# Performance work log

Measured on AMD Instinct MI355X. Metric: run time of the kernel, lower is better.

The kernel has to match this reference:

```python
import jax, jax.numpy as jnp
import numpy as np

B_, T_, L_, M_, H_, F_ = 16, 2048, 128, 256, 512, 1024
EPS = 1e-5


def _init_reservoir(h, rng):
    # orthogonal matrix scaled inside the unit disk for a stable linear recurrence
    q, _ = np.linalg.qr(rng.standard_normal((h, h)).astype(np.float32))
    return jnp.asarray(0.95 * q, dtype=jnp.float32)


def setup_inputs() -> dict:
    key = jax.random.key(0)
    ks = jax.random.split(key, 8)
    rng = np.random.default_rng(0)
    s = lambda fan_in: 1.0 / np.sqrt(fan_in)
    return {
        "x": jax.random.normal(ks[0], (B_, T_, L_), dtype=jnp.float32),
        "We": jax.random.uniform(ks[1], (L_, M_), jnp.float32, -s(L_), s(L_)),
        "be": jnp.zeros((M_,), jnp.float32),
        "Wb": jax.random.uniform(ks[2], (M_, H_), jnp.float32, -s(M_), s(M_)),
        "A": _init_reservoir(H_, rng),
        "Wr": jax.random.uniform(ks[3], (L_, H_), jnp.float32, -s(L_), s(L_)),
        "br": jnp.zeros((H_,), jnp.float32),
        "ln_g": jnp.ones((H_,), jnp.float32),
        "ln_b": jnp.zeros((H_,), jnp.float32),
        "W1": jax.random.uniform(ks[4], (H_, F_), jnp.float32, -s(H_), s(H_)),
        "b1": jnp.zeros((F_,), jnp.float32),
        "W2": jax.random.uniform(ks[5], (F_, H_), jnp.float32, -s(F_), s(F_)),
        "b2": jnp.zeros((H_,), jnp.float32),
    }


def reference(x, We, be, Wb, A, Wr, br, ln_g, ln_b, W1, b1, W2, b2):
    # encoder + B projection, batched over all timesteps: [B,T,H]
    Bu = (x @ We + be) @ Wb

    # sequential linear recurrence h_t = h_{t-1} @ A + Bu_t, h_0 = Bu_0
    def step(h, bu_t):
        h = h @ A + bu_t
        return h, h

    h0 = jnp.zeros((x.shape[0], A.shape[0]), x.dtype)
    _, Hs = jax.lax.scan(step, h0, jnp.swapaxes(Bu, 0, 1))  # [T,B,H]
    H_seq = jnp.swapaxes(Hs, 0, 1)  # [B,T,H]

    # residual + layer norm
    z = H_seq + (x @ Wr + br)
    mu = jnp.mean(z, axis=-1, keepdims=True)
    var = jnp.mean(jnp.square(z - mu), axis=-1, keepdims=True)
    zn = (z - mu) * jax.lax.rsqrt(var + EPS) * ln_g + ln_b

    # MLP on last timestep
    h_last = zn[:, -1, :]
    out = jax.nn.relu(h_last @ W1 + b1) @ W2 + b2
    return out
```

## Files before the change

### kernel.cpp

```cpp
#include <hip/hip_runtime.h>

#define B_  16
#define T_  2048
#define L_  128
#define H_  512
#define F_  1024
#define EPS 1e-5f

#define GP   68
#define GSM  (64 * GP * 2)

#define SS_P (512 * 512)

struct Job {
    const float* A; const float* Aaux; const float* B; const float* Add;
    float* C; float* C2;
    int M, lda, kLen, nbx, nrt, amode, nsA, ssA, nsB, ssB;
};

__device__ __forceinline__ float4 jloadA(const Job& jb, int gr, int gk) {
    if (jb.amode == 1) {
        if (gr < 128)  return *(const float4*)(jb.A + (long)gr * jb.lda + gk);
        if (gr == 128) return *(const float4*)(jb.Aaux + gk);
        return make_float4(0.f, 0.f, 0.f, 0.f);
    }
    if (jb.amode == 3) {
        int b = gr & 15, lag = gr >> 4;
        return *(const float4*)(jb.A + ((long)b * T_ + (T_ - 1 - lag)) * L_ + gk);
    }
    int row = gr;
    if (jb.amode == 2) row = ((gr >> 4) << 5) + 16 + (gr & 15);
    else if (gr >= jb.M) return make_float4(0.f, 0.f, 0.f, 0.f);
    const float* p = jb.A + (long)row * 512 + gk;
    float4 s = *(const float4*)p;
    for (int q = 1; q < jb.nsA; ++q) {
        float4 t = *(const float4*)(p + (long)q * jb.ssA);
        s.x += t.x; s.y += t.y; s.z += t.z; s.w += t.w;
    }
    return s;
}

__device__ __forceinline__ float4 jloadB(const Job& jb, int gk, int c) {
    const float* p = jb.B + (long)gk * 512 + c;
    float4 s = *(const float4*)p;
    for (int q = 1; q < jb.nsB; ++q) {
        float4 t = *(const float4*)(p + (long)q * jb.ssB);
        s.x += t.x; s.y += t.y; s.z += t.z; s.w += t.w;
    }
    return s;
}

__device__ __forceinline__ void g64run(float* sm, const Job& jb, int rel) {
    float* As = sm;
    float* Bs = sm + 64 * GP;
    const int tid = threadIdx.x, tx = tid & 15, ty = tid >> 4;
    const int bx = rel % jb.nbx;
    const int r  = rel / jb.nbx;
    const int by = r % jb.nrt;
    const int kc = r / jb.nrt;
    const int row0 = by * 64, col0 = bx * 64, kOff = kc * jb.kLen;

    float4 pa[4], pb[4];
#pragma unroll
    for (int t = 0; t < 4; ++t) {
        int f = tid + t * 256;
        pa[t] = jloadA(jb, row0 + (f >> 4), kOff + (f & 15) * 4);
        pb[t] = jloadB(jb, kOff + (f >> 4), col0 + (f & 15) * 4);
    }
    float acc[4][4] = {};
    for (int k0 = 0; k0 < jb.kLen; k0 += 64) {
        __syncthreads();
#pragma unroll
        for (int t = 0; t < 4; ++t) {
            int f = tid + t * 256;
            int ar = f >> 4, ak = (f & 15) * 4;
            As[(ak + 0) * GP + ar] = pa[t].x;
            As[(ak + 1) * GP + ar] = pa[t].y;
            As[(ak + 2) * GP + ar] = pa[t].z;
            As[(ak + 3) * GP + ar] = pa[t].w;
            *(float4*)&Bs[(f >> 4) * GP + (f & 15) * 4] = pb[t];
        }
        __syncthreads();
        int kn = k0 + 64;
        if (kn < jb.kLen) {
#pragma unroll
            for (int t = 0; t < 4; ++t) {
                int f = tid + t * 256;
                pa[t] = jloadA(jb, row0 + (f >> 4), kOff + kn + (f & 15) * 4);
                pb[t] = jloadB(jb, kOff + kn + (f >> 4), col0 + (f & 15) * 4);
            }
        }
#pragma unroll
        for (int kk = 0; kk < 64; ++kk) {
            float4 ra = *(float4*)&As[kk * GP + ty * 4];
            float4 rb = *(float4*)&Bs[kk * GP + tx * 4];
            acc[0][0] = fmaf(ra.x, rb.x, acc[0][0]);
            acc[0][1] = fmaf(ra.x, rb.y, acc[0][1]);
            acc[0][2] = fmaf(ra.x, rb.z, acc[0][2]);
            acc[0][3] = fmaf(ra.x, rb.w, acc[0][3]);
            acc[1][0] = fmaf(ra.y, rb.x, acc[1][0]);
            acc[1][1] = fmaf(ra.y, rb.y, acc[1][1]);
            acc[1][2] = fmaf(ra.y, rb.z, acc[1][2]);
            acc[1][3] = fmaf(ra.y, rb.w, acc[1][3]);
            acc[2][0] = fmaf(ra.z, rb.x, acc[2][0]);
            acc[2][1] = fmaf(ra.z, rb.y, acc[2][1]);
            acc[2][2] = fmaf(ra.z, rb.z, acc[2][2]);
            acc[2][3] = fmaf(ra.z, rb.w, acc[2][3]);
            acc[3][0] = fmaf(ra.w, rb.x, acc[3][0]);
            acc[3][1] = fmaf(ra.w, rb.y, acc[3][1]);
            acc[3][2] = fmaf(ra.w, rb.z, acc[3][2]);
            acc[3][3] = fmaf(ra.w, rb.w, acc[3][3]);
        }
    }
    long coff = (long)kc * jb.M * 512;
#pragma unroll
    for (int i = 0; i < 4; ++i) {
        int rr = row0 + ty * 4 + i;
        if (rr >= jb.M) continue;
        int c = col0 + tx * 4;
        float4 v = make_float4(acc[i][0], acc[i][1], acc[i][2], acc[i][3]);
        if (jb.amode == 2 && kc == 0) {
            long prow = (long)(((rr >> 4) << 5) + (rr & 15)) * 512;
            const float* ap = jb.Add + prow + c;
            for (int q = 0; q < jb.nsA; ++q) {
                float4 ad = *(const float4*)(ap + (long)q * jb.ssA);
                v.x += ad.x; v.y += ad.y; v.z += ad.z; v.w += ad.w;
            }
        }
        if (jb.amode == 3) {
            v.x += jb.Aaux[c]; v.y += jb.Aaux[c + 1];
            v.z += jb.Aaux[c + 2]; v.w += jb.Aaux[c + 3];
        }
        if (jb.amode == 1 && rr == 128)
            *(float4*)(jb.C2 + c) = v;
        else
            *(float4*)(jb.C + coff + (long)rr * 512 + c) = v;
    }
}

struct Pack { Job j[3]; int n0, n1; };

__global__ __launch_bounds__(256) void gstage(Pack p) {
    __shared__ float sm[GSM];
    int b = blockIdx.x, rel;
    const Job* jb;
    if (b < p.n0) { jb = &p.j[0]; rel = b; }
    else if (b < p.n0 + p.n1) { jb = &p.j[1]; rel = b - p.n0; }
    else { jb = &p.j[2]; rel = b - p.n0 - p.n1; }
    if (jb->amode == 9) {
        const float4* src = (const float4*)jb->A;
        float4* dst = (float4*)jb->C;
        int ss4 = jb->ssA >> 2;
        for (int i = rel * 256 + threadIdx.x; i < SS_P / 4; i += 32 * 256) {
            float4 s = src[i];
            for (int q = 1; q < jb->nsA; ++q) {
                float4 t = src[i + q * ss4];
                s.x += t.x; s.y += t.y; s.z += t.z; s.w += t.w;
            }
            dst[i] = s;
        }
        return;
    }
    g64run(sm, *jb, rel);
}

struct TP {
    const float* Y5s; const float* P32; const float* P64; const float* P96s;
    const float* x; const float* Wr; const float* zn; const float* W1;
    const float* h1p; const float* b1; const float* W2;
    float* outp; int nbx, kLen;
};

template <int MODE>
__device__ __forceinline__ float4 ta4(const TP& tp, int b, int gk) {
    if (MODE == 0) {
        if (gk < 1536) {
            int seg = gk >> 9, inner = gk & 511;
            const float* p = tp.Y5s + (long)((seg + 1) * 16 + b) * 512 + inner;
            float4 s = *(const float4*)p;
#pragma unroll
            for (int q = 1; q < 8; ++q) {
                float4 t = *(const float4*)(p + (long)q * 64 * 512);
                s.x += t.x; s.y += t.y; s.z += t.z; s.w += t.w;
            }
            return s;
        }
        return *(const float4*)(tp.x + ((long)b * T_ + T_ - 1) * L_ + gk - 1536);
    } else if (MODE == 1) {
        return *(const float4*)(tp.zn + (long)b * H_ + gk);
    } else {
        float4 s = *(const float4*)(tp.b1 + gk);
#pragma unroll
        for (int q = 0; q < 4; ++q) {
            float4 h = *(const float4*)(tp.h1p + (long)q * 16 * F_ + (long)b * F_ + gk);
            s.x += h.x; s.y += h.y; s.z += h.z; s.w += h.w;
        }
        return make_float4(fmaxf(s.x, 0.f), fmaxf(s.y, 0.f),
                           fmaxf(s.z, 0.f), fmaxf(s.w, 0.f));
    }
}

template <int MODE>
__device__ __forceinline__ float4 tb4(const TP& tp, int kr, int c) {
    if (MODE == 0) {
        if (kr < 512)  return *(const float4*)(tp.P32 + (long)kr * 512 + c);
        if (kr < 1024) return *(const float4*)(tp.P64 + (long)(kr - 512) * 512 + c);
        if (kr < 1536) {
            const float* p = tp.P96s + (long)(kr - 1024) * 512 + c;
            float4 s = *(const float4*)p;
#pragma unroll
            for (int q = 1; q < 4; ++q) {
                float4 t = *(const float4*)(p + (long)q * SS_P);
                s.x += t.x; s.y += t.y; s.z += t.z; s.w += t.w;
            }
            return s;
        }
        return *(const float4*)(tp.Wr + (long)(kr - 1536) * 512 + c);
    } else if (MODE == 1) {
        return *(const float4*)(tp.W1 + (long)kr * F_ + c);
    } else {
        return *(const float4*)(tp.W2 + (long)kr * H_ + c);
    }
}

template <int MODE>
__global__ __launch_bounds__(256) void tstage(TP tp) {
    constexpr int LDC = (MODE == 1) ? F_ : H_;
    __shared__ float sm[64 * 20 + 64 * 68];
    float* As = sm;
    float* Bs = sm + 64 * 20;
    const int tid = threadIdx.x, tx = tid & 15, ty = tid >> 4;
    const int kc = blockIdx.x / tp.nbx;
    const int col0 = (blockIdx.x % tp.nbx) * 64;
    const int kOff = kc * tp.kLen;

    float4 pa, pb[4];
    pa = ta4<MODE>(tp, ty, kOff + tx * 4);
#pragma unroll
    for (int t = 0; t < 4; ++t) {
        int f = tid + t * 256;
        pb[t] = tb4<MODE>(tp, kOff + (f >> 4), col0 + (f & 15) * 4);
    }
    float acc[4] = {};
    for (int k0 = 0; k0 < tp.kLen; k0 += 64) {
        __syncthreads();
        {
            int kk = tx * 4;
            As[(kk + 0) * 20 + ty] = pa.x;
            As[(kk + 1) * 20 + ty] = pa.y;
            As[(kk + 2) * 20 + ty] = pa.z;
            As[(kk + 3) * 20 + ty] = pa.w;
        }
#pragma unroll
        for (int t = 0; t < 4; ++t) {
            int f = tid + t * 256;
            *(float4*)&Bs[(f >> 4) * 68 + (f & 15) * 4] = pb[t];
        }
        __syncthreads();
        int kn = k0 + 64;
        if (kn < tp.kLen) {
            pa = ta4<MODE>(tp, ty, kOff + kn + tx * 4);
#pragma unroll
            for (int t = 0; t < 4; ++t) {
                int f = tid + t * 256;
                pb[t] = tb4<MODE>(tp, kOff + kn + (f >> 4), col0 + (f & 15) * 4);
            }
        }
#pragma unroll
        for (int kk = 0; kk < 64; ++kk) {
            float ra = As[kk * 20 + ty];
            float4 rb = *(float4*)&Bs[kk * 68 + tx * 4];
            acc[0] = fmaf(ra, rb.x, acc[0]);
            acc[1] = fmaf(ra, rb.y, acc[1]);
            acc[2] = fmaf(ra, rb.z, acc[2]);
            acc[3] = fmaf(ra, rb.w, acc[3]);
        }
    }
    float* dst = tp.outp + (long)kc * 16 * LDC + (long)ty * LDC + col0 + tx * 4;
    *(float4*)dst = make_float4(acc[0], acc[1], acc[2], acc[3]);
}

__global__ __launch_bounds__(256) void zln(
    const float* __restrict__ zp, const float* __restrict__ Y5s,
    const float* __restrict__ br, const float* __restrict__ lng,
    const float* __restrict__ lnb, float* __restrict__ zn)
{
    __shared__ float red1[4], red2[4];
    const int b = blockIdx.x, tid = threadIdx.x;
    float z[2];
#pragma unroll
    for (int jj = 0; jj < 2; ++jj) {
        int c = tid + jj * 256;
        float s = br[c];
#pragma unroll
        for (int q = 0; q < 13; ++q) s += zp[(long)q * 16 * H_ + (long)b * H_ + c];
#pragma unroll
        for (int q = 0; q < 8; ++q) s += Y5s[(long)q * 64 * 512 + (long)b * 512 + c];
        z[jj] = s;
    }
    float s1 = z[0] + z[1];
    float s2 = z[0] * z[0] + z[1] * z[1];
#pragma unroll
    for (int off = 32; off > 0; off >>= 1) {
        s1 += __shfl_down(s1, off, 64);
        s2 += __shfl_down(s2, off, 64);
    }
    int wid = tid >> 6, lane = tid & 63;
    if (lane == 0) { red1[wid] = s1; red2[wid] = s2; }
    __syncthreads();
    float S1 = red1[0] + red1[1] + red1[2] + red1[3];
    float S2 = red2[0] + red2[1] + red2[2] + red2[3];
    float mu  = S1 * (1.0f / H_);
    float var = S2 * (1.0f / H_) - mu * mu;
    float rs  = rsqrtf(var + EPS);
#pragma unroll
    for (int jj = 0; jj < 2; ++jj) {
        int c = tid + jj * 256;
        zn[(long)b * H_ + c] = (z[jj] - mu) * rs * lng[c] + lnb[c];
    }
}

__global__ __launch_bounds__(256) void ored(
    const float* __restrict__ op, const float* __restrict__ b2,
    float* __restrict__ out)
{
    int b = blockIdx.x >> 1;
    int c = (blockIdx.x & 1) * 256 + threadIdx.x;
    float s = b2[c];
#pragma unroll
    for (int q = 0; q < 8; ++q) s += op[(long)q * 16 * H_ + (long)b * H_ + c];
    out[(long)b * H_ + c] = s;
}

extern "C" void kernel_launch(void* const* d_in, const int* in_sizes, int n_in,
                              void* d_out, int out_size, void* d_ws, size_t ws_size,
                              hipStream_t stream) {
    const float* x    = (const float*)d_in[0];
    const float* We   = (const float*)d_in[1];
    const float* be   = (const float*)d_in[2];
    const float* Wb   = (const float*)d_in[3];
    const float* Amat = (const float*)d_in[4];
    const float* Wr   = (const float*)d_in[5];
    const float* br   = (const float*)d_in[6];
    const float* lng  = (const float*)d_in[7];
    const float* lnb  = (const float*)d_in[8];
    const float* W1   = (const float*)d_in[9];
    const float* b1   = (const float*)d_in[10];
    const float* W2   = (const float*)d_in[11];
    const float* b2   = (const float*)d_in[12];
    float* out = (float*)d_out;

    float* ws   = (float*)d_ws;
    float* Wc   = ws;
    float* bc   = Wc + 128 * 512;
    float* U0   = bc + 512;
    float* Y1s  = U0 + 2048 * 512;
    float* Y2s  = Y1s + 2 * 1024 * 512;
    float* Y3s  = Y2s + 2 * 512 * 512;
    float* Y4s  = Y3s + 4 * 256 * 512;
    float* Y5s  = Y4s + 4 * 128 * 512;
    float* P2s  = Y5s + 8 * 64 * 512;
    float* P4s  = P2s + 4 * SS_P;
    float* P8s  = P4s + 4 * SS_P;
    float* P16s = P8s + 4 * SS_P;
    float* P32s = P16s + 4 * SS_P;
    float* P64s = P32s + 4 * SS_P;
    float* P96s = P64s + 4 * SS_P;
    float* P2d  = P96s + 4 * SS_P;
    float* P4d  = P2d + SS_P;
    float* P8d  = P4d + SS_P;
    float* P16d = P8d + SS_P;
    float* P32d = P16d + SS_P;
    float* P64d = P32d + SS_P;
    float* zp   = P64d + SS_P;
    float* zn   = zp + 13 * B_ * H_;
    float* h1p  = zn + B_ * H_;
    float* op   = h1p + 4 * B_ * F_;

    Job dummy = {}; dummy.amode = 9; dummy.nsA = 1; dummy.ssA = 4;
    dummy.A = Wc; dummy.C = Wc;

    {
        Pack p; p.j[2] = dummy;
        p.j[0] = {We, be, Wb, nullptr, Wc, bc, 129, 256, 256, 8, 3, 1, 1, 0, 1, 0};
        p.j[1] = {Amat, nullptr, Amat, nullptr, P2s, nullptr, 512, 512, 128, 8, 8, 0, 1, 0, 1, 0};
        p.n0 = 24; p.n1 = 256;
        gstage<<<280, 256, 0, stream>>>(p);
    }
    {
        Pack p;
        p.j[0] = {x, bc, Wc, nullptr, U0, nullptr, 2048, 0, 128, 8, 32, 3, 1, 0, 1, 0};
        p.j[1] = {P2s, nullptr, P2s, nullptr, P4s, nullptr, 512, 512, 128, 8, 8, 0, 4, SS_P, 4, SS_P};
        p.j[2] = {P2s, nullptr, nullptr, nullptr, P2d, nullptr, 512, 512, 64, 1, 1, 9, 4, SS_P, 1, 0};
        p.n0 = 256; p.n1 = 256;
        gstage<<<544, 256, 0, stream>>>(p);
    }
    {
        Pack p;
        p.j[0] = {U0, nullptr, Amat, U0, Y1s, nullptr, 1024, 512, 256, 8, 16, 2, 1, 0, 1, 0};
        p.j[1] = {P4s, nullptr, P4s, nullptr, P8s, nullptr, 512, 512, 128, 8, 8, 0, 4, SS_P, 4, SS_P};
        p.j[2] = {P4s, nullptr, nullptr, nullptr, P4d, nullptr, 512, 512, 64, 1, 1, 9, 4, SS_P, 1, 0};
        p.n0 = 256; p.n1 = 256;
        gstage<<<544, 256, 0, stream>>>(p);
    }
    {
        Pack p;
        p.j[0] = {Y1s, nullptr, P2d, Y1s, Y2s, nullptr, 512, 512, 256, 8, 8, 2, 2, 1024 * 512, 1, 0};
        p.j[1] = {P8s, nullptr, P8s, nullptr, P16s, nullptr, 512, 512, 128, 8, 8, 0, 4, SS_P, 4, SS_P};
        p.j[2] = {P8s, nullptr, nullptr, nullptr, P8d, nullptr, 512, 512, 64, 1, 1, 9, 4, SS_P, 1, 0};
        p.n0 = 128; p.n1 = 256;
        gstage<<<416, 256, 0, stream>>>(p);
    }
    {
        Pack p;
        p.j[0] = {Y2s, nullptr, P4d, Y2s, Y3s, nullptr, 256, 512, 128, 8, 4, 2, 2, 512 * 512, 1, 0};
        p.j[1] = {P16s, nullptr, P16s, nullptr, P32s, nullptr, 512, 512, 128, 8, 8, 0, 4, SS_P, 4, SS_P};
        p.j[2] = {P16s, nullptr, nullptr, nullptr, P16d, nullptr, 512, 512, 64, 1, 1, 9, 4, SS_P, 1, 0};
        p.n0 = 128; p.n1 = 256;
        gstage<<<416, 256, 0, stream>>>(p);
    }
    {
        Pack p;
        p.j[0] = {Y3s, nullptr, P8d, Y3s, Y4s, nullptr, 128, 512, 128, 8, 2, 2, 4, 256 * 512, 1, 0};
        p.j[1] = {P32s, nullptr, P32s, nullptr, P64s, nullptr, 512, 512, 128, 8, 8, 0, 4, SS_P, 4, SS_P};
        p.j[2] = {P32s, nullptr, nullptr, nullptr, P32d, nullptr, 512, 512, 64, 1, 1, 9, 4, SS_P, 1, 0};
        p.n0 = 64; p.n1 = 256;
        gstage<<<352, 256, 0, stream>>>(p);
    }
    {
        Pack p;
        p.j[0] = {Y4s, nullptr, P16d, Y4s, Y5s, nullptr, 64, 512, 64, 8, 1, 2, 4, 128 * 512, 1, 0};
        p.j[1] = {P32d, nullptr, P64s, nullptr, P96s, nullptr, 512, 512, 128, 8, 8, 0, 1, 0, 4, SS_P};
        p.j[2] = {P64s, nullptr, nullptr, nullptr, P64d, nullptr, 512, 512, 64, 1, 1, 9, 4, SS_P, 1, 0};
        p.n0 = 64; p.n1 = 256;
        gstage<<<352, 256, 0, stream>>>(p);
    }
    TP tp;
    tp.Y5s = Y5s; tp.P32 = P32d; tp.P64 = P64d; tp.P96s = P96s;
    tp.x = x; tp.Wr = Wr; tp.zn = zn; tp.W1 = W1; tp.h1p = h1p;
    tp.b1 = b1; tp.W2 = W2;

    { TP t = tp; t.outp = zp; t.nbx = 8; t.kLen = 128;
      tstage<0><<<104, 256, 0, stream>>>(t); }
    zln<<<16, 256, 0, stream>>>(zp, Y5s, br, lng, lnb, zn);
    { TP t = tp; t.outp = h1p; t.nbx = 16; t.kLen = 128;
      tstage<1><<<64, 256, 0, stream>>>(t); }
    { TP t = tp; t.outp = op; t.nbx = 8; t.kLen = 128;
      tstage<2><<<64, 256, 0, stream>>>(t); }
    ored<<<32, 256, 0, stream>>>(op, b2, out);
}
```

Measured before the change: 342.8 us.

## Drop split-K for matrix-power chain and double split-K in tail GEMMs

The A-power squaring GEMMs (P2, P4, ..., P96) now each run as one full-K job with 64 blocks, where before they used 4-way split-K with partial buffers. That removes the separate reduction jobs and the multi-slice summation on every operand load, which shortens gstage and the Pack struct. The tail GEMMs (tstage 0/1/2) go from K chunks of 128 to 64, doubling their block counts, and the downstream reductions (zln, tstage<2> loads, ored) now sum twice as many partials. The trade-off is fewer blocks and longer serial K loops in the critical power chain, in exchange for less memory traffic and fewer reduction passes.

```diff
diff --git a/kernel.cpp b/kernel.cpp
--- a/kernel.cpp
+++ b/kernel.cpp
@@ -10,12 +10,10 @@
 #define GP   68
 #define GSM  (64 * GP * 2)
 
-#define SS_P (512 * 512)
-
 struct Job {
     const float* A; const float* Aaux; const float* B; const float* Add;
     float* C; float* C2;
-    int M, lda, kLen, nbx, nrt, amode, nsA, ssA, nsB, ssB;
+    int M, lda, kLen, nbx, nrt, amode, nsA, ssA;
 };
 
 __device__ __forceinline__ float4 jloadA(const Job& jb, int gr, int gk) {
@@ -35,16 +33,6 @@
     float4 s = *(const float4*)p;
     for (int q = 1; q < jb.nsA; ++q) {
         float4 t = *(const float4*)(p + (long)q * jb.ssA);
-        s.x += t.x; s.y += t.y; s.z += t.z; s.w += t.w;
-    }
-    return s;
-}
-
-__device__ __forceinline__ float4 jloadB(const Job& jb, int gk, int c) {
-    const float* p = jb.B + (long)gk * 512 + c;
-    float4 s = *(const float4*)p;
-    for (int q = 1; q < jb.nsB; ++q) {
-        float4 t = *(const float4*)(p + (long)q * jb.ssB);
         s.x += t.x; s.y += t.y; s.z += t.z; s.w += t.w;
     }
     return s;
@@ -65,7 +53,7 @@
     for (int t = 0; t < 4; ++t) {
         int f = tid + t * 256;
         pa[t] = jloadA(jb, row0 + (f >> 4), kOff + (f & 15) * 4);
-        pb[t] = jloadB(jb, kOff + (f >> 4), col0 + (f & 15) * 4);
+        pb[t] = *(const float4*)(jb.B + (long)(kOff + (f >> 4)) * 512 + col0 + (f & 15) * 4);
     }
     float acc[4][4] = {};
     for (int k0 = 0; k0 < jb.kLen; k0 += 64) {
@@ -87,7 +75,8 @@
             for (int t = 0; t < 4; ++t) {
                 int f = tid + t * 256;
                 pa[t] = jloadA(jb, row0 + (f >> 4), kOff + kn + (f & 15) * 4);
-                pb[t] = jloadB(jb, kOff + kn + (f >> 4), col0 + (f & 15) * 4);
+                pb[t] = *(const float4*)(jb.B + (long)(kOff + kn + (f >> 4)) * 512 +
+                                         col0 + (f & 15) * 4);
             }
         }
 #pragma unroll
@@ -138,34 +127,17 @@
     }
 }
 
-struct Pack { Job j[3]; int n0, n1; };
+struct Pack { Job j[2]; int n0; };
 
 __global__ __launch_bounds__(256) void gstage(Pack p) {
     __shared__ float sm[GSM];
-    int b = blockIdx.x, rel;
-    const Job* jb;
-    if (b < p.n0) { jb = &p.j[0]; rel = b; }
-    else if (b < p.n0 + p.n1) { jb = &p.j[1]; rel = b - p.n0; }
-    else { jb = &p.j[2]; rel = b - p.n0 - p.n1; }
-    if (jb->amode == 9) {
-        const float4* src = (const float4*)jb->A;
-        float4* dst = (float4*)jb->C;
-        int ss4 = jb->ssA >> 2;
-        for (int i = rel * 256 + threadIdx.x; i < SS_P / 4; i += 32 * 256) {
-            float4 s = src[i];
-            for (int q = 1; q < jb->nsA; ++q) {
-                float4 t = src[i + q * ss4];
-                s.x += t.x; s.y += t.y; s.z += t.z; s.w += t.w;
-            }
-            dst[i] = s;
-        }
-        return;
-    }
-    g64run(sm, *jb, rel);
+    int b = blockIdx.x;
+    if (b < p.n0) g64run(sm, p.j[0], b);
+    else          g64run(sm, p.j[1], b - p.n0);
 }
 
 struct TP {
-    const float* Y5s; const float* P32; const float* P64; const float* P96s;
+    const float* Y5s; const float* P32; const float* P64; const float* P96;
     const float* x; const float* Wr; const float* zn; const float* W1;
     const float* h1p; const float* b1; const float* W2;
     float* outp; int nbx, kLen;
@@ -191,7 +163,7 @@
     } else {
         float4 s = *(const float4*)(tp.b1 + gk);
 #pragma unroll
-        for (int q = 0; q < 4; ++q) {
+        for (int q = 0; q < 8; ++q) {
             float4 h = *(const float4*)(tp.h1p + (long)q * 16 * F_ + (long)b * F_ + gk);
             s.x += h.x; s.y += h.y; s.z += h.z; s.w += h.w;
         }
@@ -205,16 +177,7 @@
     if (MODE == 0) {
         if (kr < 512)  return *(const float4*)(tp.P32 + (long)kr * 512 + c);
         if (kr < 1024) return *(const float4*)(tp.P64 + (long)(kr - 512) * 512 + c);
-        if (kr < 1536) {
-            const float* p = tp.P96s + (long)(kr - 1024) * 512 + c;
-            float4 s = *(const float4*)p;
-#pragma unroll
-            for (int q = 1; q < 4; ++q) {
-                float4 t = *(const float4*)(p + (long)q * SS_P);
-                s.x += t.x; s.y += t.y; s.z += t.z; s.w += t.w;
-            }
-            return s;
-        }
+        if (kr < 1536) return *(const float4*)(tp.P96 + (long)(kr - 1024) * 512 + c);
         return *(const float4*)(tp.Wr + (long)(kr - 1536) * 512 + c);
     } else if (MODE == 1) {
         return *(const float4*)(tp.W1 + (long)kr * F_ + c);
@@ -293,7 +256,7 @@
         int c = tid + jj * 256;
         float s = br[c];
 #pragma unroll
-        for (int q = 0; q < 13; ++q) s += zp[(long)q * 16 * H_ + (long)b * H_ + c];
+        for (int q = 0; q < 26; ++q) s += zp[(long)q * 16 * H_ + (long)b * H_ + c];
 #pragma unroll
         for (int q = 0; q < 8; ++q) s += Y5s[(long)q * 64 * 512 + (long)b * 512 + c];
         z[jj] = s;
@@ -328,7 +291,7 @@
     int c = (blockIdx.x & 1) * 256 + threadIdx.x;
     float s = b2[c];
 #pragma unroll
-    for (int q = 0; q < 8; ++q) s += op[(long)q * 16 * H_ + (long)b * H_ + c];
+    for (int q = 0; q < 16; ++q) s += op[(long)q * 16 * H_ + (long)b * H_ + c];
     out[(long)b * H_ + c] = s;
 }
 
@@ -350,102 +313,87 @@
     const float* b2   = (const float*)d_in[12];
     float* out = (float*)d_out;
 
-    float* ws   = (float*)d_ws;
-    float* Wc   = ws;
-    float* bc   = Wc + 128 * 512;
-    float* U0   = bc + 512;
-    float* Y1s  = U0 + 2048 * 512;
-    float* Y2s  = Y1s + 2 * 1024 * 512;
-    float* Y3s  = Y2s + 2 * 512 * 512;
-    float* Y4s  = Y3s + 4 * 256 * 512;
-    float* Y5s  = Y4s + 4 * 128 * 512;
-    float* P2s  = Y5s + 8 * 64 * 512;
-    float* P4s  = P2s + 4 * SS_P;
-    float* P8s  = P4s + 4 * SS_P;
-    float* P16s = P8s + 4 * SS_P;
-    float* P32s = P16s + 4 * SS_P;
-    float* P64s = P32s + 4 * SS_P;
-    float* P96s = P64s + 4 * SS_P;
-    float* P2d  = P96s + 4 * SS_P;
-    float* P4d  = P2d + SS_P;
-    float* P8d  = P4d + SS_P;
-    float* P16d = P8d + SS_P;
-    float* P32d = P16d + SS_P;
-    float* P64d = P32d + SS_P;
-    float* zp   = P64d + SS_P;
-    float* zn   = zp + 13 * B_ * H_;
-    float* h1p  = zn + B_ * H_;
-    float* op   = h1p + 4 * B_ * F_;
-
-    Job dummy = {}; dummy.amode = 9; dummy.nsA = 1; dummy.ssA = 4;
-    dummy.A = Wc; dummy.C = Wc;
-
-    {
-        Pack p; p.j[2] = dummy;
-        p.j[0] = {We, be, Wb, nullptr, Wc, bc, 129, 256, 256, 8, 3, 1, 1, 0, 1, 0};
-        p.j[1] = {Amat, nullptr, Amat, nullptr, P2s, nullptr, 512, 512, 128, 8, 8, 0, 1, 0, 1, 0};
-        p.n0 = 24; p.n1 = 256;
-        gstage<<<280, 256, 0, stream>>>(p);
-    }
-    {
-        Pack p;
-        p.j[0] = {x, bc, Wc, nullptr, U0, nullptr, 2048, 0, 128, 8, 32, 3, 1, 0, 1, 0};
-        p.j[1] = {P2s, nullptr, P2s, nullptr, P4s, nullptr, 512, 512, 128, 8, 8, 0, 4, SS_P, 4, SS_P};
-        p.j[2] = {P2s, nullptr, nullptr, nullptr, P2d, nullptr, 512, 512, 64, 1, 1, 9, 4, SS_P, 1, 0};
-        p.n0 = 256; p.n1 = 256;
-        gstage<<<544, 256, 0, stream>>>(p);
-    }
-    {
-        Pack p;
-        p.j[0] = {U0, nullptr, Amat, U0, Y1s, nullptr, 1024, 512, 256, 8, 16, 2, 1, 0, 1, 0};
-        p.j[1] = {P4s, nullptr, P4s, nullptr, P8s, nullptr, 512, 512, 128, 8, 8, 0, 4, SS_P, 4, SS_P};
-        p.j[2] = {P4s, nullptr, nullptr, nullptr, P4d, nullptr, 512, 512, 64, 1, 1, 9, 4, SS_P, 1, 0};
-        p.n0 = 256; p.n1 = 256;
-        gstage<<<544, 256, 0, stream>>>(p);
-    }
-    {
-        Pack p;
-        p.j[0] = {Y1s, nullptr, P2d, Y1s, Y2s, nullptr, 512, 512, 256, 8, 8, 2, 2, 1024 * 512, 1, 0};
-        p.j[1] = {P8s, nullptr, P8s, nullptr, P16s, nullptr, 512, 512, 128, 8, 8, 0, 4, SS_P, 4, SS_P};
-        p.j[2] = {P8s, nullptr, nullptr, nullptr, P8d, nullptr, 512, 512, 64, 1, 1, 9, 4, SS_P, 1, 0};
-        p.n0 = 128; p.n1 = 256;
-        gstage<<<416, 256, 0, stream>>>(p);
-    }
-    {
-        Pack p;
-        p.j[0] = {Y2s, nullptr, P4d, Y2s, Y3s, nullptr, 256, 512, 128, 8, 4, 2, 2, 512 * 512, 1, 0};
-        p.j[1] = {P16s, nullptr, P16s, nullptr, P32s, nullptr, 512, 512, 128, 8, 8, 0, 4, SS_P, 4, SS_P};
-        p.j[2] = {P16s, nullptr, nullptr, nullptr, P16d, nullptr, 512, 512, 64, 1, 1, 9, 4, SS_P, 1, 0};
-        p.n0 = 128; p.n1 = 256;
-        gstage<<<416, 256, 0, stream>>>(p);
-    }
-    {
-        Pack p;
-        p.j[0] = {Y3s, nullptr, P8d, Y3s, Y4s, nullptr, 128, 512, 128, 8, 2, 2, 4, 256 * 512, 1, 0};
-        p.j[1] = {P32s, nullptr, P32s, nullptr, P64s, nullptr, 512, 512, 128, 8, 8, 0, 4, SS_P, 4, SS_P};
-        p.j[2] = {P32s, nullptr, nullptr, nullptr, P32d, nullptr, 512, 512, 64, 1, 1, 9, 4, SS_P, 1, 0};
-        p.n0 = 64; p.n1 = 256;
-        gstage<<<352, 256, 0, stream>>>(p);
-    }
-    {
-        Pack p;
-        p.j[0] = {Y4s, nullptr, P16d, Y4s, Y5s, nullptr, 64, 512, 64, 8, 1, 2, 4, 128 * 512, 1, 0};
-        p.j[1] = {P32d, nullptr, P64s, nullptr, P96s, nullptr, 512, 512, 128, 8, 8, 0, 1, 0, 4, SS_P};
-        p.j[2] = {P64s, nullptr, nullptr, nullptr, P64d, nullptr, 512, 512, 64, 1, 1, 9, 4, SS_P, 1, 0};
-        p.n0 = 64; p.n1 = 256;
-        gstage<<<352, 256, 0, stream>>>(p);
+    float* ws  = (float*)d_ws;
+    float* Wc  = ws;
+    float* bc  = Wc + 128 * 512;
+    float* U0  = bc + 512;
+    float* Y1s = U0 + 2048 * 512;
+    float* Y2s = Y1s + 2 * 1024 * 512;
+    float* Y3s = Y2s + 2 * 512 * 512;
+    float* Y4s = Y3s + 4 * 256 * 512;
+    float* Y5s = Y4s + 4 * 128 * 512;
+    float* P2  = Y5s + 8 * 64 * 512;
+    float* P4  = P2 + 512 * 512;
+    float* P8  = P4 + 512 * 512;
+    float* P16 = P8 + 512 * 512;
+    float* P32 = P16 + 512 * 512;
+    float* P64 = P32 + 512 * 512;
+    float* P96 = P64 + 512 * 512;
+    float* zp  = P96 + 512 * 512;
+    float* zn  = zp + 26 * B_ * H_;
+    float* h1p = zn + B_ * H_;
+    float* op  = h1p + 8 * B_ * F_;
+
+    {
+        Pack p;
+        p.j[0] = {We, be, Wb, nullptr, Wc, bc, 129, 256, 256, 8, 3, 1, 1, 0};
+        p.j[1] = {Amat, nullptr, Amat, nullptr, P2, nullptr, 512, 512, 512, 8, 8, 0, 1, 0};
+        p.n0 = 24;
+        gstage<<<88, 256, 0, stream>>>(p);
+    }
+    {
+        Pack p;
+        p.j[0] = {x, bc, Wc, nullptr, U0, nullptr, 2048, 0, 128, 8, 32, 3, 1, 0};
+        p.j[1] = {P2, nullptr, P2, nullptr, P4, nullptr, 512, 512, 512, 8, 8, 0, 1, 0};
+        p.n0 = 256;
+        gstage<<<320, 256, 0, stream>>>(p);
+    }
+    {
+        Pack p;
+        p.j[0] = {U0, nullptr, Amat, U0, Y1s, nullptr, 1024, 512, 256, 8, 16, 2, 1, 0};
+        p.j[1] = {P4, nullptr, P4, nullptr, P8, nullptr, 512, 512, 512, 8, 8, 0, 1, 0};
+        p.n0 = 256;
+        gstage<<<320, 256, 0, stream>>>(p);
+    }
+    {
+        Pack p;
+        p.j[0] = {Y1s, nullptr, P2, Y1s, Y2s, nullptr, 512, 512, 256, 8, 8, 2, 2, 1024 * 512};
+        p.j[1] = {P8, nullptr, P8, nullptr, P16, nullptr, 512, 512, 512, 8, 8, 0, 1, 0};
+        p.n0 = 128;
+        gstage<<<192, 256, 0, stream>>>(p);
+    }
+    {
+        Pack p;
+        p.j[0] = {Y2s, nullptr, P4, Y2s, Y3s, nullptr, 256, 512, 128, 8, 4, 2, 2, 512 * 512};
+        p.j[1] = {P16, nullptr, P16, nullptr, P32, nullptr, 512, 512, 512, 8, 8, 0, 1, 0};
+        p.n0 = 128;
+        gstage<<<192, 256, 0, stream>>>(p);
+    }
+    {
+        Pack p;
+        p.j[0] = {Y3s, nullptr, P8, Y3s, Y4s, nullptr, 128, 512, 128, 8, 2, 2, 4, 256 * 512};
+        p.j[1] = {P32, nullptr, P32, nullptr, P64, nullptr, 512, 512, 512, 8, 8, 0, 1, 0};
+        p.n0 = 64;
+        gstage<<<128, 256, 0, stream>>>(p);
+    }
+    {
+        Pack p;
+        p.j[0] = {Y4s, nullptr, P16, Y4s, Y5s, nullptr, 64, 512, 64, 8, 1, 2, 4, 128 * 512};
+        p.j[1] = {P32, nullptr, P64, nullptr, P96, nullptr, 512, 512, 512, 8, 8, 0, 1, 0};
+        p.n0 = 64;
+        gstage<<<128, 256, 0, stream>>>(p);
     }
     TP tp;
-    tp.Y5s = Y5s; tp.P32 = P32d; tp.P64 = P64d; tp.P96s = P96s;
+    tp.Y5s = Y5s; tp.P32 = P32; tp.P64 = P64; tp.P96 = P96;
     tp.x = x; tp.Wr = Wr; tp.zn = zn; tp.W1 = W1; tp.h1p = h1p;
     tp.b1 = b1; tp.W2 = W2;
 
-    { TP t = tp; t.outp = zp; t.nbx = 8; t.kLen = 128;
-      tstage<0><<<104, 256, 0, stream>>>(t); }
+    { TP t = tp; t.outp = zp; t.nbx = 8; t.kLen = 64;
+      tstage<0><<<208, 256, 0, stream>>>(t); }
     zln<<<16, 256, 0, stream>>>(zp, Y5s, br, lng, lnb, zn);
-    { TP t = tp; t.outp = h1p; t.nbx = 16; t.kLen = 128;
-      tstage<1><<<64, 256, 0, stream>>>(t); }
-    { TP t = tp; t.outp = op; t.nbx = 8; t.kLen = 128;
-      tstage<2><<<64, 256, 0, stream>>>(t); }
+    { TP t = tp; t.outp = h1p; t.nbx = 16; t.kLen = 64;
+      tstage<1><<<128, 256, 0, stream>>>(t); }
+    { TP t = tp; t.outp = op; t.nbx = 8; t.kLen = 64;
+      tstage<2><<<128, 256, 0, stream>>>(t); }
     ored<<<32, 256, 0, stream>>>(op, b2, out);
 }
```

Measured after the change: 371.6 us. 1.08x slower.
